# Kernel tuning notes

Measured on AMD Instinct MI355X. Metric: run time of the kernel, lower is better.

Reference implementation:

```python
import jax, jax.numpy as jnp
import numpy as np

_EPS = 1e-5  # torch BatchNorm2d default eps; inference mode, running_mean=0, running_var=1


def _conv1x1(x, w):
    # x: (B, C, N, K), w: (O, C) -> (B, O, N, K)  (1x1 Conv2d, no bias)
    return jnp.einsum('bcnk,oc->bonk', x, w)


def _bn(x, g, b):
    s = (g / jnp.sqrt(1.0 + _EPS))[None, :, None, None]
    return x * s + b[None, :, None, None]


def _conv_bn_relu(x, w, g, b):
    return jax.nn.relu(_bn(_conv1x1(x, w), g, b))


def _gather_neighbour(pc, idx):
    # pc: (B, N, d), idx: (B, N, K) -> (B, N, K, d)
    return jax.vmap(lambda p, i: p[i])(pc, idx)


def _att_pool(feat, fc_w, mlp_w, g, b):
    # feat: (B, C, N, K); softmax over neighbor axis K (dim=3 in torch)
    scores = jax.nn.softmax(_conv1x1(feat, fc_w), axis=3)
    agg = jnp.sum(feat * scores, axis=3, keepdims=True)  # (B, C, N, 1)
    return _conv_bn_relu(agg, mlp_w, g, b)


def setup_inputs() -> dict:
    B, N, K, d_in, d_out = 2, 32768, 16, 32, 64
    h = d_out // 2
    key = jax.random.key(0)
    ks = jax.random.split(key, 16)
    s = 0.05
    rn = lambda k, shape: jax.random.normal(ks[k], shape, dtype=jnp.float32) * s
    ones = lambda n: jnp.ones((n,), jnp.float32)
    zeros = lambda n: jnp.zeros((n,), jnp.float32)
    return {
        'feature': jax.random.normal(ks[0], (B, d_in, N, 1), dtype=jnp.float32),
        'xyz': jax.random.normal(ks[1], (B, N, 3), dtype=jnp.float32),
        'w_mlp1': rn(3, (h, d_in)), 'g_mlp1': ones(h), 'b_mlp1': zeros(h),
        'bb_w1': rn(4, (h, 10)), 'bb_g1': ones(h), 'bb_b1': zeros(h),
        'att1_fc': rn(5, (d_out, d_out)), 'att1_w': rn(6, (h, d_out)), 'att1_g': ones(h), 'att1_b': zeros(h),
        'bb_w2': rn(7, (h, h)), 'bb_g2': ones(h), 'bb_b2': zeros(h),
        'att2_fc': rn(8, (d_out, d_out)), 'att2_w': rn(9, (d_out, d_out)), 'att2_g': ones(d_out), 'att2_b': zeros(d_out),
        'w_mlp2': rn(10, (2 * d_out, d_out)), 'g_mlp2': ones(2 * d_out), 'b_mlp2': zeros(2 * d_out),
        'w_sc': rn(11, (2 * d_out, d_in)), 'g_sc': ones(2 * d_out), 'b_sc': zeros(2 * d_out),
        'neigh_idx': jax.random.randint(ks[2], (B, N, K), 0, N),
    }


def reference(feature, xyz, w_mlp1, g_mlp1, b_mlp1, bb_w1, bb_g1, bb_b1,
              att1_fc, att1_w, att1_g, att1_b, bb_w2, bb_g2, bb_b2,
              att2_fc, att2_w, att2_g, att2_b, w_mlp2, g_mlp2, b_mlp2,
              w_sc, g_sc, b_sc, neigh_idx):
    B, N, K = neigh_idx.shape
    # Dilated_res_block.mlp1
    f_pc = _conv_bn_relu(feature, w_mlp1, g_mlp1, b_mlp1)  # (B, d/2, N, 1)
    # Building_block.relative_pos_encoding
    n_xyz = _gather_neighbour(xyz, neigh_idx)                      # (B, N, K, 3)
    xyz_tile = jnp.broadcast_to(xyz[:, :, None, :], (B, N, K, 3))
    rel = xyz_tile - n_xyz
    dist = jnp.sqrt(jnp.sum(rel * rel, axis=-1, keepdims=True))
    f_xyz = jnp.concatenate([dist, rel, xyz_tile, n_xyz], axis=-1)  # (B, N, K, 10)
    f_xyz = f_xyz.transpose(0, 3, 1, 2)                             # (B, 10, N, K)
    f_xyz = _conv_bn_relu(f_xyz, bb_w1, bb_g1, bb_b1)               # (B, d/2, N, K)
    # first neighbor gather + attentive pool
    f_nb = _gather_neighbour(f_pc[:, :, :, 0].transpose(0, 2, 1), neigh_idx).transpose(0, 3, 1, 2)
    f_agg = _att_pool(jnp.concatenate([f_nb, f_xyz], axis=1), att1_fc, att1_w, att1_g, att1_b)
    # second stage
    f_xyz = _conv_bn_relu(f_xyz, bb_w2, bb_g2, bb_b2)
    f_nb = _gather_neighbour(f_agg[:, :, :, 0].transpose(0, 2, 1), neigh_idx).transpose(0, 3, 1, 2)
    f_agg = _att_pool(jnp.concatenate([f_nb, f_xyz], axis=1), att2_fc, att2_w, att2_g, att2_b)  # (B, d, N, 1)
    # Dilated_res_block.mlp2 (no activation) + shortcut + leaky relu
    f_out = _bn(_conv1x1(f_agg, w_mlp2), g_mlp2, b_mlp2)
    sc = _bn(_conv1x1(feature, w_sc), g_sc, b_sc)
    return jax.nn.leaky_relu(f_out + sc, negative_slope=0.2)  # (B, 2d, N, 1)
```

## Files before the change

### kernel.cpp

```cpp
#include <hip/hip_runtime.h>
#include <math.h>

#define NPTS 32768
#define NB 2
#define CIN 32
#define H 32
#define D 64
#define DOUT 128
#define BN_RS 0.99999500003749981f
#define LOG2E 1.44269504088896341f

typedef __attribute__((ext_vector_type(8))) short bf16x8;
typedef __attribute__((ext_vector_type(4))) short bf16x4;
typedef __attribute__((ext_vector_type(4))) float f32x4;

__device__ __forceinline__ ushort f2b(float f) {
    union { float f; unsigned u; } v; v.f = f;
    unsigned r = v.u + 0x7fffu + ((v.u >> 16) & 1u);
    return (ushort)(r >> 16);
}
__device__ __forceinline__ float b2f(ushort u) {
    union { unsigned u; float f; } v; v.u = ((unsigned)u) << 16; return v.f;
}
__device__ __forceinline__ unsigned pk2(float f0, float f1) {
    unsigned r;
    asm("v_cvt_pk_bf16_f32 %0, %1, %2" : "=v"(r) : "v"(f0), "v"(f1));
    return r;
}
__device__ __forceinline__ float qdiv(unsigned u) {
    float q = __builtin_bit_cast(float, u << 16);
    float e = __builtin_bit_cast(float, u & 0xffff0000u);
    return __fdividef(q, e);
}
__device__ __forceinline__ float ex2(float x) {
    float r; asm("v_exp_f32 %0, %1" : "=v"(r) : "v"(x)); return r;
}
__device__ __forceinline__ float xsum16(float x) {
    float a = x, b = x;
    asm("v_permlane16_swap_b32 %0, %1" : "+v"(a), "+v"(b));
    return a + b;
}
__device__ __forceinline__ float xsum32(float x) {
    float a = x, b = x;
    asm("v_permlane32_swap_b32 %0, %1" : "+v"(a), "+v"(b));
    return a + b;
}
#define MF(a, b, c) __builtin_amdgcn_mfma_f32_16x16x32_bf16(a, b, c, 0, 0, 0)

#define WBX(mi, ni, A) { uint2 _w;                                                \
    _w.x = pk2(fmaxf(A[0], 0.f), fmaxf(A[1], 0.f));                               \
    _w.y = pk2(fmaxf(A[2], 0.f), fmaxf(A[3], 0.f));                               \
    *(uint2*)&feat[wid][(ni) * 16 + c16][32 + (mi) * 16 + g4] = _w; }

#define ATT_CG(ni, cg, F0, F1) {                                                  \
    f32x4 ac = zf4;                                                               \
    ac = MF(a0_, F0, ac);                                                         \
    ac = MF(a1_, F1, ac);                                                         \
    float e0 = ex2(ac[0]), e1 = ex2(ac[1]), e2 = ex2(ac[2]), e3 = ex2(ac[3]);     \
    float E = (e0 + e1) + (e2 + e3);                                              \
    float f0 = b2f(feat[wid][(ni) * 16 + g4 + 0][(cg) * 16 + c16]);               \
    float f1 = b2f(feat[wid][(ni) * 16 + g4 + 1][(cg) * 16 + c16]);               \
    float f2 = b2f(feat[wid][(ni) * 16 + g4 + 2][(cg) * 16 + c16]);               \
    float f3 = b2f(feat[wid][(ni) * 16 + g4 + 3][(cg) * 16 + c16]);               \
    float Q = e0 * f0; Q = fmaf(e1, f1, Q); Q = fmaf(e2, f2, Q); Q = fmaf(e3, f3, Q); \
    E = xsum32(xsum16(E));                                                        \
    Q = xsum32(xsum16(Q));                                                        \
    if (g == 0) qe[(wid << 2) + (ni)][(cg) * 16 + c16] = pk2(Q, E); }
#define ATT_NI(ni) {                                                              \
    bf16x8 a0_ = *(const bf16x8*)&feat[wid][(ni) * 16 + c16][g8];                 \
    bf16x8 a1_ = *(const bf16x8*)&feat[wid][(ni) * 16 + c16][32 + g8];            \
    ATT_CG(ni, 0, afc0_0, afc0_1) ATT_CG(ni, 1, afc1_0, afc1_1)                   \
    ATT_CG(ni, 2, afc2_0, afc2_1) ATT_CG(ni, 3, afc3_0, afc3_1) }

#define QFRAG(bbv, base) {                                                        \
    uint4 _qa = *(const uint4*)&qe[c16][(base) + g8];                             \
    uint4 _qb = *(const uint4*)&qe[c16][(base) + g8 + 4];                         \
    bbv.u.x = pk2(qdiv(_qa.x), qdiv(_qa.y));                                      \
    bbv.u.y = pk2(qdiv(_qa.z), qdiv(_qa.w));                                      \
    bbv.u.z = pk2(qdiv(_qb.x), qdiv(_qb.y));                                      \
    bbv.u.w = pk2(qdiv(_qb.z), qdiv(_qb.w)); }

__global__ __launch_bounds__(256, 4) void k1_mlp1(
    const float* __restrict__ feature, const float* __restrict__ w_mlp1,
    const float* __restrict__ g_mlp1, const float* __restrict__ b_mlp1,
    ushort* __restrict__ f_pc, ushort* __restrict__ featpm)
{
    int tid = threadIdx.x;
    int pg = blockIdx.x * 256 + tid;
    int b = pg >> 15, n = pg & (NPTS - 1);

    float x[CIN];
#pragma unroll
    for (int c = 0; c < CIN; ++c)
        x[c] = feature[((b * CIN + c) << 15) + n];

    float outv[CIN];
#pragma unroll
    for (int o = 0; o < CIN; ++o) {
        float s0 = 0.f, s1 = 0.f, s2 = 0.f, s3 = 0.f;
        const float* w = w_mlp1 + o * CIN;
#pragma unroll
        for (int c = 0; c < CIN; c += 4) {
            s0 = fmaf(w[c + 0], x[c + 0], s0);
            s1 = fmaf(w[c + 1], x[c + 1], s1);
            s2 = fmaf(w[c + 2], x[c + 2], s2);
            s3 = fmaf(w[c + 3], x[c + 3], s3);
        }
        float acc = (s0 + s1) + (s2 + s3);
        outv[o] = fmaxf(fmaf(acc, g_mlp1[o] * BN_RS, b_mlp1[o]), 0.f);
    }
    uint4* dst = (uint4*)(f_pc + ((size_t)pg << 5));
    uint4* dst2 = (uint4*)(featpm + ((size_t)pg << 5));
#pragma unroll
    for (int j = 0; j < 4; ++j) {
        uint4 u;
        u.x = pk2(outv[8 * j + 0], outv[8 * j + 1]);
        u.y = pk2(outv[8 * j + 2], outv[8 * j + 3]);
        u.z = pk2(outv[8 * j + 4], outv[8 * j + 5]);
        u.w = pk2(outv[8 * j + 6], outv[8 * j + 7]);
        dst[j] = u;
        uint4 v;
        v.x = pk2(x[8 * j + 0], x[8 * j + 1]);
        v.y = pk2(x[8 * j + 2], x[8 * j + 3]);
        v.z = pk2(x[8 * j + 4], x[8 * j + 5]);
        v.w = pk2(x[8 * j + 6], x[8 * j + 7]);
        dst2[j] = v;
    }
}

__global__ __launch_bounds__(256, 3) void k2_stage1(
    const float* __restrict__ xyz, const int* __restrict__ nidx,
    const ushort* __restrict__ f_pc,
    const float* __restrict__ bb_w1, const float* __restrict__ bb_g1, const float* __restrict__ bb_b1,
    const float* __restrict__ att_fc,
    const float* __restrict__ att_w, const float* __restrict__ att_g, const float* __restrict__ att_b,
    ushort* __restrict__ f_agg)
{
    __shared__ __align__(16) ushort feat[4][64][72];
    __shared__ __align__(16) unsigned qe[16][68];
    __shared__ __align__(16) ushort fcb[64][72];
    __shared__ __align__(16) ushort w1p[32][40];

    int tid = threadIdx.x;
    for (int i = tid; i < D * D; i += 256) fcb[i >> 6][i & 63] = f2b(att_fc[i] * LOG2E);
    for (int i = tid; i < 32 * 32; i += 256) {
        int o = i >> 5, k = i & 31;
        w1p[o][k] = (k < 10) ? f2b(bb_w1[o * 10 + k] * (bb_g1[o] * BN_RS)) : (ushort)0;
    }
    __syncthreads();

    int wid = tid >> 6, lane = tid & 63;
    int g = lane >> 4, c16 = lane & 15;
    int g4 = g << 2, g8 = g << 3;
    f32x4 zf4 = {0.f, 0.f, 0.f, 0.f};

    int pb = (blockIdx.x << 4) + (wid << 2) + g;
    int b = pb >> 15, n = pb & (NPTS - 1);
    int nb = nidx[((size_t)pb << 4) + c16];

    const bf16x8* gsrc = (const bf16x8*)(f_pc + (((size_t)(b * NPTS + nb)) << 5));
    bf16x8 gv0 = gsrc[0], gv1 = gsrc[1], gv2 = gsrc[2], gv3 = gsrc[3];

    const float* cx = xyz + (size_t)(b * NPTS + n) * 3;
    const float* nx = xyz + (size_t)(b * NPTS + nb) * 3;
    float c0 = cx[0], c1 = cx[1], c2 = cx[2];
    float x0 = nx[0], x1 = nx[1], x2 = nx[2];
    float r0 = c0 - x0, r1 = c1 - x1, r2 = c2 - x2;
    float dist = sqrtf(r0 * r0 + r1 * r1 + r2 * r2);

    {
        uint4 u0; u0.x = pk2(dist, r0); u0.y = pk2(r1, r2); u0.z = pk2(c0, c1); u0.w = pk2(c2, x0);
        uint4 u1; u1.x = pk2(x1, x2); u1.y = 0; u1.z = 0; u1.w = 0;
        uint4 z4; z4.x = 0; z4.y = 0; z4.z = 0; z4.w = 0;
        *(uint4*)&feat[wid][lane][32] = u0;
        *(uint4*)&feat[wid][lane][40] = u1;
        *(uint4*)&feat[wid][lane][48] = z4;
        *(uint4*)&feat[wid][lane][56] = z4;
    }
    {
        bf16x8 xb0 = *(const bf16x8*)&feat[wid][ 0 + c16][32 + g8];
        bf16x8 xb1 = *(const bf16x8*)&feat[wid][16 + c16][32 + g8];
        bf16x8 xb2 = *(const bf16x8*)&feat[wid][32 + c16][32 + g8];
        bf16x8 xb3 = *(const bf16x8*)&feat[wid][48 + c16][32 + g8];
        bf16x8 wa0 = *(const bf16x8*)&w1p[     c16][g8];
        bf16x8 wa1 = *(const bf16x8*)&w1p[16 + c16][g8];
        f32x4 bi0 = *(const f32x4*)&bb_b1[g4];
        f32x4 bi1 = *(const f32x4*)&bb_b1[16 + g4];
        f32x4 f00 = MF(wa0, xb0, bi0);
        f32x4 f01 = MF(wa0, xb1, bi0);
        f32x4 f02 = MF(wa0, xb2, bi0);
        f32x4 f03 = MF(wa0, xb3, bi0);
        f32x4 f10 = MF(wa1, xb0, bi1);
        f32x4 f11 = MF(wa1, xb1, bi1);
        f32x4 f12 = MF(wa1, xb2, bi1);
        f32x4 f13 = MF(wa1, xb3, bi1);
        WBX(0, 0, f00) WBX(0, 1, f01) WBX(0, 2, f02) WBX(0, 3, f03)
        WBX(1, 0, f10) WBX(1, 1, f11) WBX(1, 2, f12) WBX(1, 3, f13)
    }
    *(bf16x8*)&feat[wid][lane][0]  = gv0;
    *(bf16x8*)&feat[wid][lane][8]  = gv1;
    *(bf16x8*)&feat[wid][lane][16] = gv2;
    *(bf16x8*)&feat[wid][lane][24] = gv3;

    bf16x8 afc0_0 = *(const bf16x8*)&fcb[ 0 + c16][     g8];
    bf16x8 afc0_1 = *(const bf16x8*)&fcb[ 0 + c16][32 + g8];
    bf16x8 afc1_0 = *(const bf16x8*)&fcb[16 + c16][     g8];
    bf16x8 afc1_1 = *(const bf16x8*)&fcb[16 + c16][32 + g8];
    bf16x8 afc2_0 = *(const bf16x8*)&fcb[32 + c16][     g8];
    bf16x8 afc2_1 = *(const bf16x8*)&fcb[32 + c16][32 + g8];
    bf16x8 afc3_0 = *(const bf16x8*)&fcb[48 + c16][     g8];
    bf16x8 afc3_1 = *(const bf16x8*)&fcb[48 + c16][32 + g8];

    ATT_NI(0) ATT_NI(1) ATT_NI(2) ATT_NI(3)
    __syncthreads();

    if (wid < 2) {
        union { bf16x8 v; uint4 u; } bb0, bb1;
        QFRAG(bb0, 0)
        QFRAG(bb1, 32)
        int o = (wid << 4) + c16;
        float sc = att_g[o] * BN_RS;
        const float* wr0 = att_w + o * D + g8;
        const float* wr1 = att_w + o * D + 32 + g8;
        union { bf16x8 v; uint4 u; } aw0, aw1;
        aw0.u.x = pk2(wr0[0] * sc, wr0[1] * sc);
        aw0.u.y = pk2(wr0[2] * sc, wr0[3] * sc);
        aw0.u.z = pk2(wr0[4] * sc, wr0[5] * sc);
        aw0.u.w = pk2(wr0[6] * sc, wr0[7] * sc);
        aw1.u.x = pk2(wr1[0] * sc, wr1[1] * sc);
        aw1.u.y = pk2(wr1[2] * sc, wr1[3] * sc);
        aw1.u.z = pk2(wr1[4] * sc, wr1[5] * sc);
        aw1.u.w = pk2(wr1[6] * sc, wr1[7] * sc);
        f32x4 acc = *(const f32x4*)&att_b[(wid << 4) + g4];
        acc = MF(aw0.v, bb0.v, acc);
        acc = MF(aw1.v, bb1.v, acc);
        int p = (blockIdx.x << 4) + c16;
        int o0 = (wid << 4) + g4;
        uint2 st;
        st.x = pk2(fmaxf(acc[0], 0.f), fmaxf(acc[1], 0.f));
        st.y = pk2(fmaxf(acc[2], 0.f), fmaxf(acc[3], 0.f));
        *(uint2*)(f_agg + (((size_t)p) << 5) + o0) = st;
    }
}

__global__ __launch_bounds__(256, 3) void k3_stage2(
    const float* __restrict__ xyz, const int* __restrict__ nidx,
    const ushort* __restrict__ f_agg,
    const float* __restrict__ bb_w1, const float* __restrict__ bb_g1, const float* __restrict__ bb_b1,
    const float* __restrict__ bb_w2, const float* __restrict__ bb_g2, const float* __restrict__ bb_b2,
    const float* __restrict__ att_fc,
    const float* __restrict__ att_w, const float* __restrict__ att_g, const float* __restrict__ att_b,
    ushort* __restrict__ fagg2b)
{
    __shared__ __align__(16) ushort feat[4][64][72];
    __shared__ __align__(16) unsigned qe[16][68];
    __shared__ __align__(16) ushort fcb[64][72];
    __shared__ __align__(16) ushort w1p[32][40];

    int tid = threadIdx.x;
    for (int i = tid; i < D * D; i += 256) fcb[i >> 6][i & 63] = f2b(att_fc[i] * LOG2E);
    for (int i = tid; i < 32 * 32; i += 256) {
        int o = i >> 5, k = i & 31;
        w1p[o][k] = (k < 10) ? f2b(bb_w1[o * 10 + k] * (bb_g1[o] * BN_RS)) : (ushort)0;
    }
    __syncthreads();

    int wid = tid >> 6, lane = tid & 63;
    int g = lane >> 4, c16 = lane & 15;
    int g4 = g << 2, g8 = g << 3;
    f32x4 zf4 = {0.f, 0.f, 0.f, 0.f};

    int pb = (blockIdx.x << 4) + (wid << 2) + g;
    int b = pb >> 15, n = pb & (NPTS - 1);
    int nb = nidx[((size_t)pb << 4) + c16];

    const bf16x8* gsrc = (const bf16x8*)(f_agg + (((size_t)(b * NPTS + nb)) << 5));
    bf16x8 gv0 = gsrc[0], gv1 = gsrc[1], gv2 = gsrc[2], gv3 = gsrc[3];

    const float* cx = xyz + (size_t)(b * NPTS + n) * 3;
    const float* nx = xyz + (size_t)(b * NPTS + nb) * 3;
    float c0 = cx[0], c1 = cx[1], c2 = cx[2];
    float x0 = nx[0], x1 = nx[1], x2 = nx[2];
    float r0 = c0 - x0, r1 = c1 - x1, r2 = c2 - x2;
    float dist = sqrtf(r0 * r0 + r1 * r1 + r2 * r2);

    {
        uint4 u0; u0.x = pk2(dist, r0); u0.y = pk2(r1, r2); u0.z = pk2(c0, c1); u0.w = pk2(c2, x0);
        uint4 u1; u1.x = pk2(x1, x2); u1.y = 0; u1.z = 0; u1.w = 0;
        uint4 z4; z4.x = 0; z4.y = 0; z4.z = 0; z4.w = 0;
        *(uint4*)&feat[wid][lane][32] = u0;
        *(uint4*)&feat[wid][lane][40] = u1;
        *(uint4*)&feat[wid][lane][48] = z4;
        *(uint4*)&feat[wid][lane][56] = z4;
    }
    {
        bf16x8 xb0 = *(const bf16x8*)&feat[wid][ 0 + c16][32 + g8];
        bf16x8 xb1 = *(const bf16x8*)&feat[wid][16 + c16][32 + g8];
        bf16x8 xb2 = *(const bf16x8*)&feat[wid][32 + c16][32 + g8];
        bf16x8 xb3 = *(const bf16x8*)&feat[wid][48 + c16][32 + g8];
        bf16x8 wa0 = *(const bf16x8*)&w1p[     c16][g8];
        bf16x8 wa1 = *(const bf16x8*)&w1p[16 + c16][g8];
        f32x4 bi0 = *(const f32x4*)&bb_b1[g4];
        f32x4 bi1 = *(const f32x4*)&bb_b1[16 + g4];
        f32x4 f00 = MF(wa0, xb0, bi0);
        f32x4 f01 = MF(wa0, xb1, bi0);
        f32x4 f02 = MF(wa0, xb2, bi0);
        f32x4 f03 = MF(wa0, xb3, bi0);
        f32x4 f10 = MF(wa1, xb0, bi1);
        f32x4 f11 = MF(wa1, xb1, bi1);
        f32x4 f12 = MF(wa1, xb2, bi1);
        f32x4 f13 = MF(wa1, xb3, bi1);
        WBX(0, 0, f00) WBX(0, 1, f01) WBX(0, 2, f02) WBX(0, 3, f03)
        WBX(1, 0, f10) WBX(1, 1, f11) WBX(1, 2, f12) WBX(1, 3, f13)
    }
    union { bf16x8 v; uint4 u; } aw20, aw21;
    {
        int o = c16;
        float sc2 = bb_g2[o] * BN_RS;
        const float* wr = bb_w2 + o * H + g8;
        aw20.u.x = pk2(wr[0] * sc2, wr[1] * sc2);
        aw20.u.y = pk2(wr[2] * sc2, wr[3] * sc2);
        aw20.u.z = pk2(wr[4] * sc2, wr[5] * sc2);
        aw20.u.w = pk2(wr[6] * sc2, wr[7] * sc2);
    }
    {
        int o = 16 + c16;
        float sc2 = bb_g2[o] * BN_RS;
        const float* wr = bb_w2 + o * H + g8;
        aw21.u.x = pk2(wr[0] * sc2, wr[1] * sc2);
        aw21.u.y = pk2(wr[2] * sc2, wr[3] * sc2);
        aw21.u.z = pk2(wr[4] * sc2, wr[5] * sc2);
        aw21.u.w = pk2(wr[6] * sc2, wr[7] * sc2);
    }
    {
        bf16x8 bfx0 = *(const bf16x8*)&feat[wid][ 0 + c16][32 + g8];
        bf16x8 bfx1 = *(const bf16x8*)&feat[wid][16 + c16][32 + g8];
        bf16x8 bfx2 = *(const bf16x8*)&feat[wid][32 + c16][32 + g8];
        bf16x8 bfx3 = *(const bf16x8*)&feat[wid][48 + c16][32 + g8];
        f32x4 bi0 = *(const f32x4*)&bb_b2[     g4];
        f32x4 bi1 = *(const f32x4*)&bb_b2[16 + g4];
        f32x4 a00 = MF(aw20.v, bfx0, bi0);
        f32x4 a01 = MF(aw20.v, bfx1, bi0);
        f32x4 a02 = MF(aw20.v, bfx2, bi0);
        f32x4 a03 = MF(aw20.v, bfx3, bi0);
        f32x4 a10 = MF(aw21.v, bfx0, bi1);
        f32x4 a11 = MF(aw21.v, bfx1, bi1);
        f32x4 a12 = MF(aw21.v, bfx2, bi1);
        f32x4 a13 = MF(aw21.v, bfx3, bi1);
        WBX(0, 0, a00) WBX(0, 1, a01) WBX(0, 2, a02) WBX(0, 3, a03)
        WBX(1, 0, a10) WBX(1, 1, a11) WBX(1, 2, a12) WBX(1, 3, a13)
    }
    *(bf16x8*)&feat[wid][lane][0]  = gv0;
    *(bf16x8*)&feat[wid][lane][8]  = gv1;
    *(bf16x8*)&feat[wid][lane][16] = gv2;
    *(bf16x8*)&feat[wid][lane][24] = gv3;

    bf16x8 afc0_0 = *(const bf16x8*)&fcb[ 0 + c16][     g8];
    bf16x8 afc0_1 = *(const bf16x8*)&fcb[ 0 + c16][32 + g8];
    bf16x8 afc1_0 = *(const bf16x8*)&fcb[16 + c16][     g8];
    bf16x8 afc1_1 = *(const bf16x8*)&fcb[16 + c16][32 + g8];
    bf16x8 afc2_0 = *(const bf16x8*)&fcb[32 + c16][     g8];
    bf16x8 afc2_1 = *(const bf16x8*)&fcb[32 + c16][32 + g8];
    bf16x8 afc3_0 = *(const bf16x8*)&fcb[48 + c16][     g8];
    bf16x8 afc3_1 = *(const bf16x8*)&fcb[48 + c16][32 + g8];

    ATT_NI(0) ATT_NI(1) ATT_NI(2) ATT_NI(3)
    __syncthreads();

    {
        union { bf16x8 v; uint4 u; } bb0, bb1;
        QFRAG(bb0, 0)
        QFRAG(bb1, 32)
        int o = (wid << 4) + c16;
        float sc = att_g[o] * BN_RS;
        const float* wr0 = att_w + o * D + g8;
        const float* wr1 = att_w + o * D + 32 + g8;
        union { bf16x8 v; uint4 u; } aw0, aw1;
        aw0.u.x = pk2(wr0[0] * sc, wr0[1] * sc);
        aw0.u.y = pk2(wr0[2] * sc, wr0[3] * sc);
        aw0.u.z = pk2(wr0[4] * sc, wr0[5] * sc);
        aw0.u.w = pk2(wr0[6] * sc, wr0[7] * sc);
        aw1.u.x = pk2(wr1[0] * sc, wr1[1] * sc);
        aw1.u.y = pk2(wr1[2] * sc, wr1[3] * sc);
        aw1.u.z = pk2(wr1[4] * sc, wr1[5] * sc);
        aw1.u.w = pk2(wr1[6] * sc, wr1[7] * sc);
        f32x4 acc = *(const f32x4*)&att_b[(wid << 4) + g4];
        acc = MF(aw0.v, bb0.v, acc);
        acc = MF(aw1.v, bb1.v, acc);
        int p = (blockIdx.x << 4) + c16;
        int o0 = (wid << 4) + g4;
        uint2 st;
        st.x = pk2(fmaxf(acc[0], 0.f), fmaxf(acc[1], 0.f));
        st.y = pk2(fmaxf(acc[2], 0.f), fmaxf(acc[3], 0.f));
        *(uint2*)(fagg2b + (((size_t)p) << 6) + o0) = st;
    }
}

__global__ __launch_bounds__(256, 4) void k4_final(
    const ushort* __restrict__ fagg2b, const ushort* __restrict__ featpm,
    const float* __restrict__ w_mlp2, const float* __restrict__ g_mlp2, const float* __restrict__ b_mlp2,
    const float* __restrict__ w_sc, const float* __restrict__ g_sc, const float* __restrict__ b_sc,
    float* __restrict__ out)
{
    int tid = threadIdx.x;
    int wid = tid >> 6, lane = tid & 63;
    int c16 = lane & 15, g = lane >> 4;
    int g4 = g << 2, g8 = g << 3;
    int p0 = blockIdx.x << 6;
    int o0 = wid << 5;

    union { bf16x8 v; uint4 u; } A[2][3];
#pragma unroll
    for (int mi = 0; mi < 2; ++mi) {
        int o = o0 + mi * 16 + c16;
        float sm = g_mlp2[o] * BN_RS, ss = g_sc[o] * BN_RS;
        const float* wm = w_mlp2 + o * D;
        const float* ws = w_sc + o * CIN;
#pragma unroll
        for (int ks = 0; ks < 2; ++ks) {
            float4 wa = *(const float4*)&wm[ks * 32 + g8];
            float4 wb = *(const float4*)&wm[ks * 32 + g8 + 4];
            A[mi][ks].u.x = pk2(wa.x * sm, wa.y * sm);
            A[mi][ks].u.y = pk2(wa.z * sm, wa.w * sm);
            A[mi][ks].u.z = pk2(wb.x * sm, wb.y * sm);
            A[mi][ks].u.w = pk2(wb.z * sm, wb.w * sm);
        }
        float4 wa = *(const float4*)&ws[g8];
        float4 wb = *(const float4*)&ws[g8 + 4];
        A[mi][2].u.x = pk2(wa.x * ss, wa.y * ss);
        A[mi][2].u.y = pk2(wa.z * ss, wa.w * ss);
        A[mi][2].u.z = pk2(wb.x * ss, wb.y * ss);
        A[mi][2].u.w = pk2(wb.z * ss, wb.w * ss);
    }
    float bias0[4], bias1[4];
#pragma unroll
    for (int r = 0; r < 4; ++r) {
        int oa = o0 + g4 + r;
        int ob = o0 + 16 + g4 + r;
        bias0[r] = b_mlp2[oa] + b_sc[oa];
        bias1[r] = b_mlp2[ob] + b_sc[ob];
    }

    int bb = p0 >> 15;
#pragma unroll
    for (int ni = 0; ni < 4; ++ni) {
        int pt = p0 + ni * 16 + c16;
        bf16x8 B0 = *(const bf16x8*)&fagg2b[((size_t)pt << 6) + g8];
        bf16x8 B1 = *(const bf16x8*)&fagg2b[((size_t)pt << 6) + 32 + g8];
        bf16x8 B2 = *(const bf16x8*)&featpm[((size_t)pt << 5) + g8];
        f32x4 acc0 = {bias0[0], bias0[1], bias0[2], bias0[3]};
        f32x4 acc1 = {bias1[0], bias1[1], bias1[2], bias1[3]};
        acc0 = MF(A[0][0].v, B0, acc0);
        acc0 = MF(A[0][1].v, B1, acc0);
        acc0 = MF(A[0][2].v, B2, acc0);
        acc1 = MF(A[1][0].v, B0, acc1);
        acc1 = MF(A[1][1].v, B1, acc1);
        acc1 = MF(A[1][2].v, B2, acc1);
        int nn = pt & (NPTS - 1);
#pragma unroll
        for (int r = 0; r < 4; ++r) {
            float v0 = acc0[r];
            v0 = (v0 >= 0.f) ? v0 : 0.2f * v0;
            out[((bb * DOUT + o0 + g4 + r) << 15) + nn] = v0;
            float v1 = acc1[r];
            v1 = (v1 >= 0.f) ? v1 : 0.2f * v1;
            out[((bb * DOUT + o0 + 16 + g4 + r) << 15) + nn] = v1;
        }
    }
}

extern "C" void kernel_launch(void* const* d_in, const int* in_sizes, int n_in,
                              void* d_out, int out_size, void* d_ws, size_t ws_size,
                              hipStream_t stream) {
    const float* feature = (const float*)d_in[0];
    const float* xyz     = (const float*)d_in[1];
    const float* w_mlp1  = (const float*)d_in[2];
    const float* g_mlp1  = (const float*)d_in[3];
    const float* b_mlp1  = (const float*)d_in[4];
    const float* bb_w1   = (const float*)d_in[5];
    const float* bb_g1   = (const float*)d_in[6];
    const float* bb_b1   = (const float*)d_in[7];
    const float* att1_fc = (const float*)d_in[8];
    const float* att1_w  = (const float*)d_in[9];
    const float* att1_g  = (const float*)d_in[10];
    const float* att1_b  = (const float*)d_in[11];
    const float* bb_w2   = (const float*)d_in[12];
    const float* bb_g2   = (const float*)d_in[13];
    const float* bb_b2   = (const float*)d_in[14];
    const float* att2_fc = (const float*)d_in[15];
    const float* att2_w  = (const float*)d_in[16];
    const float* att2_g  = (const float*)d_in[17];
    const float* att2_b  = (const float*)d_in[18];
    const float* w_mlp2  = (const float*)d_in[19];
    const float* g_mlp2  = (const float*)d_in[20];
    const float* b_mlp2  = (const float*)d_in[21];
    const float* w_sc    = (const float*)d_in[22];
    const float* g_sc    = (const float*)d_in[23];
    const float* b_sc    = (const float*)d_in[24];
    const int*   nidx    = (const int*)d_in[25];
    float* out = (float*)d_out;

    ushort* f_pc_bf  = (ushort*)d_ws;
    ushort* f_agg_bf = f_pc_bf + (size_t)NB * NPTS * 32;
    ushort* featpm   = f_agg_bf + (size_t)NB * NPTS * 32;
    ushort* fagg2b   = featpm + (size_t)NB * NPTS * 32;

    k1_mlp1<<<NB * NPTS / 256, 256, 0, stream>>>(feature, w_mlp1, g_mlp1, b_mlp1,
                                                 f_pc_bf, featpm);
    k2_stage1<<<NB * NPTS / 16, 256, 0, stream>>>(xyz, nidx, f_pc_bf,
                                                  bb_w1, bb_g1, bb_b1,
                                                  att1_fc, att1_w, att1_g, att1_b, f_agg_bf);
    k3_stage2<<<NB * NPTS / 16, 256, 0, stream>>>(xyz, nidx, f_agg_bf,
                                                  bb_w1, bb_g1, bb_b1,
                                                  bb_w2, bb_g2, bb_b2,
                                                  att2_fc, att2_w, att2_g, att2_b, fagg2b);
    k4_final<<<NB * NPTS / 64, 256, 0, stream>>>(fagg2b, featpm,
                                                 w_mlp2, g_mlp2, b_mlp2,
                                                 w_sc, g_sc, b_sc, out);
}
```

Before: 132.9 us.

## Swizzle feature LDS layout, load att_fc fragments from global, raise occupancy

```diff
diff --git a/kernel.cpp b/kernel.cpp
--- a/kernel.cpp
+++ b/kernel.cpp
@@ -47,10 +47,23 @@
 }
 #define MF(a, b, c) __builtin_amdgcn_mfma_f32_16x16x32_bf16(a, b, c, 0, 0, 0)
 
+#define FQ(row, col) ((((row)) << 6) + (((col) ^ (((row) & 7) << 3))))
+
 #define WBX(mi, ni, A) { uint2 _w;                                                \
     _w.x = pk2(fmaxf(A[0], 0.f), fmaxf(A[1], 0.f));                               \
     _w.y = pk2(fmaxf(A[2], 0.f), fmaxf(A[3], 0.f));                               \
-    *(uint2*)&feat[wid][(ni) * 16 + c16][32 + (mi) * 16 + g4] = _w; }
+    *(uint2*)&featS[wid][FQ((ni) * 16 + c16, 32 + (mi) * 16 + g4)] = _w; }
+
+#define LDA(cg, ks, DST) {                                                        \
+    const float* _wr = att_fc + ((cg) * 16 + c16) * D + (ks) * 32 + g8;           \
+    float4 _wa = *(const float4*)&_wr[0];                                         \
+    float4 _wb = *(const float4*)&_wr[4];                                         \
+    union { bf16x8 v; uint4 u; } _t;                                              \
+    _t.u.x = pk2(_wa.x * LOG2E, _wa.y * LOG2E);                                   \
+    _t.u.y = pk2(_wa.z * LOG2E, _wa.w * LOG2E);                                   \
+    _t.u.z = pk2(_wb.x * LOG2E, _wb.y * LOG2E);                                   \
+    _t.u.w = pk2(_wb.z * LOG2E, _wb.w * LOG2E);                                   \
+    DST = _t.v; }
 
 #define ATT_CG(ni, cg, F0, F1) {                                                  \
     f32x4 ac = zf4;                                                               \
@@ -58,17 +71,17 @@
     ac = MF(a1_, F1, ac);                                                         \
     float e0 = ex2(ac[0]), e1 = ex2(ac[1]), e2 = ex2(ac[2]), e3 = ex2(ac[3]);     \
     float E = (e0 + e1) + (e2 + e3);                                              \
-    float f0 = b2f(feat[wid][(ni) * 16 + g4 + 0][(cg) * 16 + c16]);               \
-    float f1 = b2f(feat[wid][(ni) * 16 + g4 + 1][(cg) * 16 + c16]);               \
-    float f2 = b2f(feat[wid][(ni) * 16 + g4 + 2][(cg) * 16 + c16]);               \
-    float f3 = b2f(feat[wid][(ni) * 16 + g4 + 3][(cg) * 16 + c16]);               \
+    float f0 = b2f(featS[wid][FQ((ni) * 16 + g4 + 0, (cg) * 16 + c16)]);          \
+    float f1 = b2f(featS[wid][FQ((ni) * 16 + g4 + 1, (cg) * 16 + c16)]);          \
+    float f2 = b2f(featS[wid][FQ((ni) * 16 + g4 + 2, (cg) * 16 + c16)]);          \
+    float f3 = b2f(featS[wid][FQ((ni) * 16 + g4 + 3, (cg) * 16 + c16)]);          \
     float Q = e0 * f0; Q = fmaf(e1, f1, Q); Q = fmaf(e2, f2, Q); Q = fmaf(e3, f3, Q); \
     E = xsum32(xsum16(E));                                                        \
     Q = xsum32(xsum16(Q));                                                        \
     if (g == 0) qe[(wid << 2) + (ni)][(cg) * 16 + c16] = pk2(Q, E); }
 #define ATT_NI(ni) {                                                              \
-    bf16x8 a0_ = *(const bf16x8*)&feat[wid][(ni) * 16 + c16][g8];                 \
-    bf16x8 a1_ = *(const bf16x8*)&feat[wid][(ni) * 16 + c16][32 + g8];            \
+    bf16x8 a0_ = *(const bf16x8*)&featS[wid][FQ((ni) * 16 + c16, g8)];            \
+    bf16x8 a1_ = *(const bf16x8*)&featS[wid][FQ((ni) * 16 + c16, 32 + g8)];       \
     ATT_CG(ni, 0, afc0_0, afc0_1) ATT_CG(ni, 1, afc1_0, afc1_1)                   \
     ATT_CG(ni, 2, afc2_0, afc2_1) ATT_CG(ni, 3, afc3_0, afc3_1) }
 
@@ -128,7 +141,7 @@
     }
 }
 
-__global__ __launch_bounds__(256, 3) void k2_stage1(
+__global__ __launch_bounds__(256, 4) void k2_stage1(
     const float* __restrict__ xyz, const int* __restrict__ nidx,
     const ushort* __restrict__ f_pc,
     const float* __restrict__ bb_w1, const float* __restrict__ bb_g1, const float* __restrict__ bb_b1,
@@ -136,13 +149,11 @@
     const float* __restrict__ att_w, const float* __restrict__ att_g, const float* __restrict__ att_b,
     ushort* __restrict__ f_agg)
 {
-    __shared__ __align__(16) ushort feat[4][64][72];
+    __shared__ __align__(16) ushort featS[4][64 * 64];
     __shared__ __align__(16) unsigned qe[16][68];
-    __shared__ __align__(16) ushort fcb[64][72];
     __shared__ __align__(16) ushort w1p[32][40];
 
     int tid = threadIdx.x;
-    for (int i = tid; i < D * D; i += 256) fcb[i >> 6][i & 63] = f2b(att_fc[i] * LOG2E);
     for (int i = tid; i < 32 * 32; i += 256) {
         int o = i >> 5, k = i & 31;
         w1p[o][k] = (k < 10) ? f2b(bb_w1[o * 10 + k] * (bb_g1[o] * BN_RS)) : (ushort)0;
@@ -172,16 +183,16 @@
         uint4 u0; u0.x = pk2(dist, r0); u0.y = pk2(r1, r2); u0.z = pk2(c0, c1); u0.w = pk2(c2, x0);
         uint4 u1; u1.x = pk2(x1, x2); u1.y = 0; u1.z = 0; u1.w = 0;
         uint4 z4; z4.x = 0; z4.y = 0; z4.z = 0; z4.w = 0;
-        *(uint4*)&feat[wid][lane][32] = u0;
-        *(uint4*)&feat[wid][lane][40] = u1;
-        *(uint4*)&feat[wid][lane][48] = z4;
-        *(uint4*)&feat[wid][lane][56] = z4;
-    }
-    {
-        bf16x8 xb0 = *(const bf16x8*)&feat[wid][ 0 + c16][32 + g8];
-        bf16x8 xb1 = *(const bf16x8*)&feat[wid][16 + c16][32 + g8];
-        bf16x8 xb2 = *(const bf16x8*)&feat[wid][32 + c16][32 + g8];
-        bf16x8 xb3 = *(const bf16x8*)&feat[wid][48 + c16][32 + g8];
+        *(uint4*)&featS[wid][FQ(lane, 32)] = u0;
+        *(uint4*)&featS[wid][FQ(lane, 40)] = u1;
+        *(uint4*)&featS[wid][FQ(lane, 48)] = z4;
+        *(uint4*)&featS[wid][FQ(lane, 56)] = z4;
+    }
+    {
+        bf16x8 xb0 = *(const bf16x8*)&featS[wid][FQ( 0 + c16, 32 + g8)];
+        bf16x8 xb1 = *(const bf16x8*)&featS[wid][FQ(16 + c16, 32 + g8)];
+        bf16x8 xb2 = *(const bf16x8*)&featS[wid][FQ(32 + c16, 32 + g8)];
+        bf16x8 xb3 = *(const bf16x8*)&featS[wid][FQ(48 + c16, 32 + g8)];
         bf16x8 wa0 = *(const bf16x8*)&w1p[     c16][g8];
         bf16x8 wa1 = *(const bf16x8*)&w1p[16 + c16][g8];
         f32x4 bi0 = *(const f32x4*)&bb_b1[g4];
@@ -197,19 +208,16 @@
         WBX(0, 0, f00) WBX(0, 1, f01) WBX(0, 2, f02) WBX(0, 3, f03)
         WBX(1, 0, f10) WBX(1, 1, f11) WBX(1, 2, f12) WBX(1, 3, f13)
     }
-    *(bf16x8*)&feat[wid][lane][0]  = gv0;
-    *(bf16x8*)&feat[wid][lane][8]  = gv1;
-    *(bf16x8*)&feat[wid][lane][16] = gv2;
-    *(bf16x8*)&feat[wid][lane][24] = gv3;
-
-    bf16x8 afc0_0 = *(const bf16x8*)&fcb[ 0 + c16][     g8];
-    bf16x8 afc0_1 = *(const bf16x8*)&fcb[ 0 + c16][32 + g8];
-    bf16x8 afc1_0 = *(const bf16x8*)&fcb[16 + c16][     g8];
-    bf16x8 afc1_1 = *(const bf16x8*)&fcb[16 + c16][32 + g8];
-    bf16x8 afc2_0 = *(const bf16x8*)&fcb[32 + c16][     g8];
-    bf16x8 afc2_1 = *(const bf16x8*)&fcb[32 + c16][32 + g8];
-    bf16x8 afc3_0 = *(const bf16x8*)&fcb[48 + c16][     g8];
-    bf16x8 afc3_1 = *(const bf16x8*)&fcb[48 + c16][32 + g8];
+    *(bf16x8*)&featS[wid][FQ(lane, 0)]  = gv0;
+    *(bf16x8*)&featS[wid][FQ(lane, 8)]  = gv1;
+    *(bf16x8*)&featS[wid][FQ(lane, 16)] = gv2;
+    *(bf16x8*)&featS[wid][FQ(lane, 24)] = gv3;
+
+    bf16x8 afc0_0, afc0_1, afc1_0, afc1_1, afc2_0, afc2_1, afc3_0, afc3_1;
+    LDA(0, 0, afc0_0) LDA(0, 1, afc0_1)
+    LDA(1, 0, afc1_0) LDA(1, 1, afc1_1)
+    LDA(2, 0, afc2_0) LDA(2, 1, afc2_1)
+    LDA(3, 0, afc3_0) LDA(3, 1, afc3_1)
 
     ATT_NI(0) ATT_NI(1) ATT_NI(2) ATT_NI(3)
     __syncthreads();
@@ -243,7 +251,7 @@
     }
 }
 
-__global__ __launch_bounds__(256, 3) void k3_stage2(
+__global__ __launch_bounds__(256, 4) void k3_stage2(
     const float* __restrict__ xyz, const int* __restrict__ nidx,
     const ushort* __restrict__ f_agg,
     const float* __restrict__ bb_w1, const float* __restrict__ bb_g1, const float* __restrict__ bb_b1,
@@ -252,13 +260,11 @@
     const float* __restrict__ att_w, const float* __restrict__ att_g, const float* __restrict__ att_b,
     ushort* __restrict__ fagg2b)
 {
-    __shared__ __align__(16) ushort feat[4][64][72];
+    __shared__ __align__(16) ushort featS[4][64 * 64];
     __shared__ __align__(16) unsigned qe[16][68];
-    __shared__ __align__(16) ushort fcb[64][72];
     __shared__ __align__(16) ushort w1p[32][40];
 
     int tid = threadIdx.x;
-    for (int i = tid; i < D * D; i += 256) fcb[i >> 6][i & 63] = f2b(att_fc[i] * LOG2E);
     for (int i = tid; i < 32 * 32; i += 256) {
         int o = i >> 5, k = i & 31;
         w1p[o][k] = (k < 10) ? f2b(bb_w1[o * 10 + k] * (bb_g1[o] * BN_RS)) : (ushort)0;
@@ -288,16 +294,16 @@
         uint4 u0; u0.x = pk2(dist, r0); u0.y = pk2(r1, r2); u0.z = pk2(c0, c1); u0.w = pk2(c2, x0);
         uint4 u1; u1.x = pk2(x1, x2); u1.y = 0; u1.z = 0; u1.w = 0;
         uint4 z4; z4.x = 0; z4.y = 0; z4.z = 0; z4.w = 0;
-        *(uint4*)&feat[wid][lane][32] = u0;
-        *(uint4*)&feat[wid][lane][40] = u1;
-        *(uint4*)&feat[wid][lane][48] = z4;
-        *(uint4*)&feat[wid][lane][56] = z4;
-    }
-    {
-        bf16x8 xb0 = *(const bf16x8*)&feat[wid][ 0 + c16][32 + g8];
-        bf16x8 xb1 = *(const bf16x8*)&feat[wid][16 + c16][32 + g8];
-        bf16x8 xb2 = *(const bf16x8*)&feat[wid][32 + c16][32 + g8];
-        bf16x8 xb3 = *(const bf16x8*)&feat[wid][48 + c16][32 + g8];
+        *(uint4*)&featS[wid][FQ(lane, 32)] = u0;
+        *(uint4*)&featS[wid][FQ(lane, 40)] = u1;
+        *(uint4*)&featS[wid][FQ(lane, 48)] = z4;
+        *(uint4*)&featS[wid][FQ(lane, 56)] = z4;
+    }
+    {
+        bf16x8 xb0 = *(const bf16x8*)&featS[wid][FQ( 0 + c16, 32 + g8)];
+        bf16x8 xb1 = *(const bf16x8*)&featS[wid][FQ(16 + c16, 32 + g8)];
+        bf16x8 xb2 = *(const bf16x8*)&featS[wid][FQ(32 + c16, 32 + g8)];
+        bf16x8 xb3 = *(const bf16x8*)&featS[wid][FQ(48 + c16, 32 + g8)];
         bf16x8 wa0 = *(const bf16x8*)&w1p[     c16][g8];
         bf16x8 wa1 = *(const bf16x8*)&w1p[16 + c16][g8];
         f32x4 bi0 = *(const f32x4*)&bb_b1[g4];
@@ -333,10 +339,10 @@
         aw21.u.w = pk2(wr[6] * sc2, wr[7] * sc2);
     }
     {
-        bf16x8 bfx0 = *(const bf16x8*)&feat[wid][ 0 + c16][32 + g8];
-        bf16x8 bfx1 = *(const bf16x8*)&feat[wid][16 + c16][32 + g8];
-        bf16x8 bfx2 = *(const bf16x8*)&feat[wid][32 + c16][32 + g8];
-        bf16x8 bfx3 = *(const bf16x8*)&feat[wid][48 + c16][32 + g8];
+        bf16x8 bfx0 = *(const bf16x8*)&featS[wid][FQ( 0 + c16, 32 + g8)];
+        bf16x8 bfx1 = *(const bf16x8*)&featS[wid][FQ(16 + c16, 32 + g8)];
+        bf16x8 bfx2 = *(const bf16x8*)&featS[wid][FQ(32 + c16, 32 + g8)];
+        bf16x8 bfx3 = *(const bf16x8*)&featS[wid][FQ(48 + c16, 32 + g8)];
         f32x4 bi0 = *(const f32x4*)&bb_b2[     g4];
         f32x4 bi1 = *(const f32x4*)&bb_b2[16 + g4];
         f32x4 a00 = MF(aw20.v, bfx0, bi0);
@@ -350,19 +356,16 @@
         WBX(0, 0, a00) WBX(0, 1, a01) WBX(0, 2, a02) WBX(0, 3, a03)
         WBX(1, 0, a10) WBX(1, 1, a11) WBX(1, 2, a12) WBX(1, 3, a13)
     }
-    *(bf16x8*)&feat[wid][lane][0]  = gv0;
-    *(bf16x8*)&feat[wid][lane][8]  = gv1;
-    *(bf16x8*)&feat[wid][lane][16] = gv2;
-    *(bf16x8*)&feat[wid][lane][24] = gv3;
-
-    bf16x8 afc0_0 = *(const bf16x8*)&fcb[ 0 + c16][     g8];
-    bf16x8 afc0_1 = *(const bf16x8*)&fcb[ 0 + c16][32 + g8];
-    bf16x8 afc1_0 = *(const bf16x8*)&fcb[16 + c16][     g8];
-    bf16x8 afc1_1 = *(const bf16x8*)&fcb[16 + c16][32 + g8];
-    bf16x8 afc2_0 = *(const bf16x8*)&fcb[32 + c16][     g8];
-    bf16x8 afc2_1 = *(const bf16x8*)&fcb[32 + c16][32 + g8];
-    bf16x8 afc3_0 = *(const bf16x8*)&fcb[48 + c16][     g8];
-    bf16x8 afc3_1 = *(const bf16x8*)&fcb[48 + c16][32 + g8];
+    *(bf16x8*)&featS[wid][FQ(lane, 0)]  = gv0;
+    *(bf16x8*)&featS[wid][FQ(lane, 8)]  = gv1;
+    *(bf16x8*)&featS[wid][FQ(lane, 16)] = gv2;
+    *(bf16x8*)&featS[wid][FQ(lane, 24)] = gv3;
+
+    bf16x8 afc0_0, afc0_1, afc1_0, afc1_1, afc2_0, afc2_1, afc3_0, afc3_1;
+    LDA(0, 0, afc0_0) LDA(0, 1, afc0_1)
+    LDA(1, 0, afc1_0) LDA(1, 1, afc1_1)
+    LDA(2, 0, afc2_0) LDA(2, 1, afc2_1)
+    LDA(3, 0, afc3_0) LDA(3, 1, afc3_1)
 
     ATT_NI(0) ATT_NI(1) ATT_NI(2) ATT_NI(3)
     __syncthreads();
```

Measured after the change: 161.0 us. 21.2% more time.
